# Kernel optimization log

Measured on AMD Instinct MI355X. Metric: run time of the kernel, lower is better.

## Reference

```python
import jax, jax.numpy as jnp
import numpy as np

B, S, C = 256, 169, 512      # batch, input seq_len (hardcoded 169 in source), n_attn
H, TT, HS = 256, 256, 16     # n_head, ctx_len, head_size (all forced by hardcoded shapes)
OUT = 64                     # output Linear(16, 64)


def setup_inputs() -> dict:
    key = jax.random.key(0)
    ks = jax.random.split(key, 13)
    s_in = 1.0 / np.sqrt(C)
    s_hs = 1.0 / np.sqrt(HS)
    return {
        "x": jax.random.normal(ks[0], (B, S, C), dtype=jnp.float32),
        "time_w": jax.random.normal(ks[1], (H, TT), dtype=jnp.float32) * 0.1,
        "time_alpha": jax.random.normal(ks[2], (H, 1, TT), dtype=jnp.float32) * 0.1 + 1.0,
        "time_beta": jax.random.normal(ks[3], (H, TT, 1), dtype=jnp.float32) * 0.1 + 1.0,
        "time_gamma": jax.random.normal(ks[4], (TT, 1), dtype=jnp.float32) * 0.1 + 1.0,
        "key_w": jax.random.normal(ks[5], (HS, C), dtype=jnp.float32) * s_in,
        "key_b": jax.random.normal(ks[6], (HS,), dtype=jnp.float32) * s_in,
        "value_w": jax.random.normal(ks[7], (HS, C), dtype=jnp.float32) * s_in,
        "value_b": jax.random.normal(ks[8], (HS,), dtype=jnp.float32) * s_in,
        "recep_w": jax.random.normal(ks[9], (HS, C), dtype=jnp.float32) * s_in,
        "recep_b": jax.random.normal(ks[10], (HS,), dtype=jnp.float32) * s_in,
        "out_w": jax.random.normal(ks[11], (OUT, HS), dtype=jnp.float32) * s_hs,
        "out_b": jax.random.normal(ks[12], (OUT,), dtype=jnp.float32) * s_hs,
    }


def reference(x, time_w, time_alpha, time_beta, time_gamma,
              key_w, key_b, value_w, value_b, recep_w, recep_b,
              out_w, out_b):
    # --- build the time-decay matrix via the pad/tile shift trick ---
    w = jnp.pad(time_w, ((0, 0), (0, TT)))            # (H, 2TT)
    w = jnp.tile(w, (1, TT))                          # (H, 2TT*TT)
    w = w[:, :-TT].reshape(H, TT, 2 * TT - 1)
    w = w[:, :, TT - 1:]                              # (H, TT, TT)
    w = w * time_alpha * time_beta                    # (H, TT, TT)

    # --- channel-half time shift: first C/2 channels shifted back by 1 step ---
    half = C // 2
    shifted = jnp.pad(x[:, :, :half], ((0, 0), (1, 0), (0, 0)))[:, :-1]
    x = jnp.concatenate([shifted, x[:, :, half:]], axis=-1)

    # --- projections (torch Linear: y = x @ W.T + b) ---
    k = x @ key_w.T + key_b                           # (B, S, HS)
    v = x @ value_w.T + value_b
    r = x @ recep_w.T + recep_b

    pad_len = TT - S                                  # 256 - 169 = 87
    r = jnp.pad(r, ((0, 0), (0, pad_len), (0, 0)))    # (B, TT, HS)

    k = jnp.exp(jnp.clip(k, -60.0, 30.0))
    sum_k = jnp.cumsum(k, axis=1)                     # (B, S, HS)
    sum_k = jnp.pad(sum_k, ((0, 0), (0, pad_len), (0, 0)))  # (B, TT, HS)

    kv = k * v                                        # (B, S, HS)
    kv = jnp.pad(kv, ((0, 0), (0, pad_len), (0, 0)))  # (B, TT, HS)

    # einsum('htu,bhc->btc') == contract u first, then (t,h) matmul against kv's seq axis
    w2 = w.sum(axis=-1)                               # (H, TT): sum_u w[h,t,u]
    wkv = jnp.einsum('ht,bhc->btc', w2, kv)           # (B, TT, HS)

    # original divides by zero-padded sum_k in the padded tail; guard with 1 there
    denom = jnp.where(sum_k == 0, jnp.ones_like(sum_k), sum_k)
    rwkv = jax.nn.sigmoid(r) * wkv / denom            # (B, TT, HS)

    rwkv = rwkv @ out_w.T + out_b                     # (B, TT, 64)
    rwkv = rwkv * time_gamma[:TT]                     # (TT,1) broadcast
    return rwkv
```

## Files before the change

kernel.cpp:

```cpp
#include <hip/hip_runtime.h>

typedef unsigned short u16;
typedef unsigned int u32;
typedef __attribute__((ext_vector_type(8))) __bf16 bf16x8;
typedef __attribute__((ext_vector_type(8))) u16 u16x8;
typedef __attribute__((ext_vector_type(4))) float f32x4;

#define S_LEN 169
#define C_DIM 512
#define SP 192

#define WT_OFF  0
#define XT_OFF  49152
#define KE_OFF  0
#define KVF_OFF 11264
#define RF_OFF  22528
#define KVT_OFF 33792
#define G_OFF   39936
#define RB_OFF  51200
#define SS_OFF  71680
#define OW_OFF  72704
#define LDS_BYTES 77824

__device__ __forceinline__ u16 f2b(float f) {
    union { float f; u32 u; } v; v.f = f;
    u32 u = v.u;
    return (u16)((u + 0x7fffu + ((u >> 16) & 1u)) >> 16);
}

__global__ __launch_bounds__(256) void w2_kernel(
    const float* __restrict__ time_w,
    const float* __restrict__ time_alpha,
    const float* __restrict__ time_beta,
    u16* __restrict__ w2t)
{
    __shared__ float tw[256];
    __shared__ float al[256];
    const int s = blockIdx.x;
    const int t = threadIdx.x;
    if (s >= S_LEN) { w2t[t * SP + s] = 0; return; }
    tw[t] = time_w[s * 256 + t];
    al[t] = time_alpha[s * 256 + t];
    __syncthreads();
    float acc = 0.f;
    for (int u = 0; u <= t; ++u)
        acc = fmaf(tw[255 + u - t], al[u], acc);
    w2t[t * SP + s] = f2b(time_beta[s * 256 + t] * acc);
}

__global__ __launch_bounds__(512) void rwkv_main(
    const float* __restrict__ x,
    const float* __restrict__ key_w, const float* __restrict__ key_b,
    const float* __restrict__ value_w, const float* __restrict__ value_b,
    const float* __restrict__ recep_w, const float* __restrict__ recep_b,
    const float* __restrict__ out_w, const float* __restrict__ out_b,
    const float* __restrict__ gamma,
    const u16* __restrict__ w2t,
    float* __restrict__ out)
{
    __shared__ __align__(16) char smem[LDS_BYTES];
    const int tid  = threadIdx.x;
    const int lane = tid & 63;
    const int wid  = tid >> 6;
    const int q    = lane >> 4;
    const int hs   = lane & 15;
    const int b    = blockIdx.x;
    const float* xb = x + (size_t)b * (S_LEN * C_DIM);

    for (int i = tid; i < 3072; i += 512) {
        int j  = i >> 6;
        int co = (i & 63) << 3;
        const float* src;
        if (j < 16)      src = key_w   + j * 512 + co;
        else if (j < 32) src = value_w + (j - 16) * 512 + co;
        else             src = recep_w + (j - 32) * 512 + co;
        float4 f0 = *(const float4*)src;
        float4 f1 = *(const float4*)(src + 4);
        u16x8 p;
        p[0]=f2b(f0.x); p[1]=f2b(f0.y); p[2]=f2b(f0.z); p[3]=f2b(f0.w);
        p[4]=f2b(f1.x); p[5]=f2b(f1.y); p[6]=f2b(f1.z); p[7]=f2b(f1.w);
        u32 off = (((u32)j << 10) + ((u32)co << 1)) ^ (((u32)(j & 7)) << 4);
        *(u16x8*)(smem + WT_OFF + off) = p;
    }

    const float kb = key_b[hs];
    const float vb = value_b[hs];
    const float rb = recep_b[hs];

    f32x4 acc0[3], acc1[3];
    #pragma unroll
    for (int n = 0; n < 3; ++n) { acc0[n] = (f32x4){0.f,0.f,0.f,0.f}; acc1[n] = (f32x4){0.f,0.f,0.f,0.f}; }
    const bool has_m1 = (wid < 3);

    for (int chunk = 0; chunk < 8; ++chunk) {
        if (chunk) __syncthreads();
        const bool shifted = chunk < 4;
        for (int i = tid; i < 1408; i += 512) {
            int r  = i >> 3;
            int co = (i & 7) << 3;
            int cg = (chunk << 6) + co;
            int tsrc = shifted ? (r - 1) : r;
            bool valid = shifted ? (r >= 1 && r <= S_LEN) : (r < S_LEN);
            u16x8 p = {0,0,0,0,0,0,0,0};
            if (valid) {
                const float* src = xb + (size_t)tsrc * C_DIM + cg;
                float4 f0 = *(const float4*)src;
                float4 f1 = *(const float4*)(src + 4);
                p[0]=f2b(f0.x); p[1]=f2b(f0.y); p[2]=f2b(f0.z); p[3]=f2b(f0.w);
                p[4]=f2b(f1.x); p[5]=f2b(f1.y); p[6]=f2b(f1.z); p[7]=f2b(f1.w);
            }
            u32 off = (((u32)r << 7) + ((u32)co << 1)) ^ (((u32)(r & 7)) << 4);
            *(u16x8*)(smem + XT_OFF + off) = p;
        }
        __syncthreads();
        #pragma unroll
        for (int ks = 0; ks < 2; ++ks) {
            int kc = ks << 5;
            bf16x8 bfr[3];
            #pragma unroll
            for (int nt = 0; nt < 3; ++nt) {
                int j = nt * 16 + hs;
                u32 col = (u32)((chunk << 6) + kc + (q << 3));
                u32 off = (((u32)j << 10) + (col << 1)) ^ (((u32)(j & 7)) << 4);
                bfr[nt] = *(const bf16x8*)(smem + WT_OFF + off);
            }
            {
                int row = wid * 16 + hs;
                u32 off = (((u32)row << 7) + ((u32)(kc + (q << 3)) << 1)) ^ (((u32)(row & 7)) << 4);
                bf16x8 afr = *(const bf16x8*)(smem + XT_OFF + off);
                acc0[0] = __builtin_amdgcn_mfma_f32_16x16x32_bf16(afr, bfr[0], acc0[0], 0,0,0);
                acc0[1] = __builtin_amdgcn_mfma_f32_16x16x32_bf16(afr, bfr[1], acc0[1], 0,0,0);
                acc0[2] = __builtin_amdgcn_mfma_f32_16x16x32_bf16(afr, bfr[2], acc0[2], 0,0,0);
            }
            if (has_m1) {
                int row = (wid + 8) * 16 + hs;
                u32 off = (((u32)row << 7) + ((u32)(kc + (q << 3)) << 1)) ^ (((u32)(row & 7)) << 4);
                bf16x8 afr = *(const bf16x8*)(smem + XT_OFF + off);
                acc1[0] = __builtin_amdgcn_mfma_f32_16x16x32_bf16(afr, bfr[0], acc1[0], 0,0,0);
                acc1[1] = __builtin_amdgcn_mfma_f32_16x16x32_bf16(afr, bfr[1], acc1[1], 0,0,0);
                acc1[2] = __builtin_amdgcn_mfma_f32_16x16x32_bf16(afr, bfr[2], acc1[2], 0,0,0);
            }
        }
    }
    __syncthreads();

    float* kef = (float*)(smem + KE_OFF);
    float* kvf = (float*)(smem + KVF_OFF);
    float* rff = (float*)(smem + RF_OFF);
    #pragma unroll
    for (int m = 0; m < 2; ++m) {
        if (m == 1 && !has_m1) break;
        const f32x4* A = (m == 0) ? acc0 : acc1;
        int tb = (wid + m * 8) * 16 + (q << 2);
        float ke[4];
        #pragma unroll
        for (int rg = 0; rg < 4; ++rg) {
            float kk = A[0][rg] + kb;
            kk = fminf(fmaxf(kk, -60.f), 30.f);
            ke[rg] = __expf(kk);
        }
        #pragma unroll
        for (int rg = 0; rg < 4; ++rg) {
            int t = tb + rg;
            kef[t * 16 + hs] = ke[rg];
            kvf[t * 16 + hs] = ke[rg] * (A[1][rg] + vb);
            rff[t * 16 + hs] = A[2][rg] + rb;
        }
    }
    __syncthreads();

    float* seg = (float*)(smem + SS_OFF);
    float* g   = (float*)(smem + G_OFF);
    if (tid < 256) {
        int h = tid & 15, sg = tid >> 4;
        int t0 = sg * 11, t1 = (t0 + 11 < S_LEN) ? t0 + 11 : S_LEN;
        float s = 0.f;
        for (int t = t0; t < t1; ++t) s += kef[t * 16 + h];
        seg[sg * 16 + h] = s;
    } else {
        int i2 = tid - 256;
        for (int i = i2; i < 4096; i += 256) {
            int row = i >> 4, c = 16 + (i & 15);
            ((u16*)(smem + RB_OFF))[row * 40 + c] = 0;
        }
        for (int i = i2; i < 368; i += 256) {
            int h = i & 15; int t = S_LEN + (i >> 4);
            u32 off = ((u32)(h * 384 + t * 2)) ^ (((u32)(h & 7)) << 4);
            *(u16*)(smem + KVT_OFF + off) = 0;
        }
        for (int i = i2; i < 2560; i += 256) {
            int o = i / 40, c = i - o * 40;
            u16 vb16 = (c < 16) ? f2b(out_w[o * 16 + c]) : (u16)0;
            ((u16*)(smem + OW_OFF))[o * 40 + c] = vb16;
        }
    }
    __syncthreads();
    if (tid < 16) {
        float run = 0.f;
        for (int sg = 0; sg < 16; ++sg) {
            float v = seg[sg * 16 + tid];
            seg[sg * 16 + tid] = run;
            run += v;
        }
    }
    __syncthreads();
    if (tid < 256) {
        int h = tid & 15, sg = tid >> 4;
        int t0 = sg * 11, t1 = (t0 + 11 < S_LEN) ? t0 + 11 : S_LEN;
        float run = seg[sg * 16 + h];
        for (int t = t0; t < t1; ++t) {
            run += kef[t * 16 + h];
            u32 off = ((u32)(h * 384 + t * 2)) ^ (((u32)(h & 7)) << 4);
            *(u16*)(smem + KVT_OFF + off) = f2b(kvf[t * 16 + h]);
            float rr = rff[t * 16 + h];
            float sig = 1.f / (1.f + __expf(-rr));
            g[t * 16 + h] = sig / run;
        }
    }
    __syncthreads();

    f32x4 wa0 = (f32x4){0.f,0.f,0.f,0.f};
    f32x4 wa1 = (f32x4){0.f,0.f,0.f,0.f};
    #pragma unroll
    for (int s0 = 0; s0 < SP; s0 += 32) {
        int scol = s0 + (q << 3);
        u32 boff = ((u32)(hs * 384 + scol * 2)) ^ (((u32)(hs & 7)) << 4);
        bf16x8 bfr = *(const bf16x8*)(smem + KVT_OFF + boff);
        {
            int row = wid * 16 + hs;
            bf16x8 afr = *(const bf16x8*)(w2t + row * SP + scol);
            wa0 = __builtin_amdgcn_mfma_f32_16x16x32_bf16(afr, bfr, wa0, 0,0,0);
        }
        {
            int row = (wid + 8) * 16 + hs;
            bf16x8 afr = *(const bf16x8*)(w2t + row * SP + scol);
            wa1 = __builtin_amdgcn_mfma_f32_16x16x32_bf16(afr, bfr, wa1, 0,0,0);
        }
    }
    #pragma unroll
    for (int m = 0; m < 2; ++m) {
        const f32x4& W = (m == 0) ? wa0 : wa1;
        int tb = (wid + m * 8) * 16 + (q << 2);
        #pragma unroll
        for (int rg = 0; rg < 4; ++rg) {
            int t = tb + rg;
            float fac = (t < S_LEN) ? g[t * 16 + hs] : 0.5f;
            ((u16*)(smem + RB_OFF))[t * 40 + hs] = f2b(W[rg] * fac);
        }
    }
    __syncthreads();

    float obv[4];
    #pragma unroll
    for (int nt = 0; nt < 4; ++nt) obv[nt] = out_b[nt * 16 + hs];
    #pragma unroll
    for (int m = 0; m < 2; ++m) {
        int mt = wid + m * 8;
        int arow = mt * 16 + hs;
        bf16x8 afr = *(const bf16x8*)(smem + RB_OFF + (u32)(arow * 80 + (q << 4)));
        float gm[4];
        #pragma unroll
        for (int rg = 0; rg < 4; ++rg) gm[rg] = gamma[mt * 16 + (q << 2) + rg];
        #pragma unroll
        for (int nt = 0; nt < 4; ++nt) {
            int orow = nt * 16 + hs;
            bf16x8 bfr = *(const bf16x8*)(smem + OW_OFF + (u32)(orow * 80 + (q << 4)));
            f32x4 zc = (f32x4){0.f,0.f,0.f,0.f};
            f32x4 d = __builtin_amdgcn_mfma_f32_16x16x32_bf16(afr, bfr, zc, 0,0,0);
            #pragma unroll
            for (int rg = 0; rg < 4; ++rg) {
                int t = mt * 16 + (q << 2) + rg;
                out[(size_t)b * 16384 + (size_t)t * 64 + nt * 16 + hs] = (d[rg] + obv[nt]) * gm[rg];
            }
        }
    }
}

extern "C" void kernel_launch(void* const* d_in, const int* in_sizes, int n_in,
                              void* d_out, int out_size, void* d_ws, size_t ws_size,
                              hipStream_t stream) {
    const float* x          = (const float*)d_in[0];
    const float* time_w     = (const float*)d_in[1];
    const float* time_alpha = (const float*)d_in[2];
    const float* time_beta  = (const float*)d_in[3];
    const float* time_gamma = (const float*)d_in[4];
    const float* key_w      = (const float*)d_in[5];
    const float* key_b      = (const float*)d_in[6];
    const float* value_w    = (const float*)d_in[7];
    const float* value_b    = (const float*)d_in[8];
    const float* recep_w    = (const float*)d_in[9];
    const float* recep_b    = (const float*)d_in[10];
    const float* out_w      = (const float*)d_in[11];
    const float* out_b      = (const float*)d_in[12];
    u16* w2t = (u16*)d_ws;

    w2_kernel<<<192, 256, 0, stream>>>(time_w, time_alpha, time_beta, w2t);
    rwkv_main<<<256, 512, 0, stream>>>(x, key_w, key_b, value_w, value_b,
                                       recep_w, recep_b, out_w, out_b,
                                       time_gamma, w2t, (float*)d_out);
}
```

Measured before the change: 40.91 us.

## Double-buffer x chunks in LDS with register prefetch; split w2 reduction

```diff
diff --git a/kernel.cpp b/kernel.cpp
--- a/kernel.cpp
+++ b/kernel.cpp
@@ -3,7 +3,6 @@
 typedef unsigned short u16;
 typedef unsigned int u32;
 typedef __attribute__((ext_vector_type(8))) __bf16 bf16x8;
-typedef __attribute__((ext_vector_type(8))) u16 u16x8;
 typedef __attribute__((ext_vector_type(4))) float f32x4;
 
 #define S_LEN 169
@@ -11,7 +10,8 @@
 #define SP 192
 
 #define WT_OFF  0
-#define XT_OFF  49152
+#define XT0_OFF 49152
+#define XT1_OFF 71680
 #define KE_OFF  0
 #define KVF_OFF 11264
 #define RF_OFF  22528
@@ -20,32 +20,36 @@
 #define RB_OFF  51200
 #define SS_OFF  71680
 #define OW_OFF  72704
-#define LDS_BYTES 77824
-
-__device__ __forceinline__ u16 f2b(float f) {
-    union { float f; u32 u; } v; v.f = f;
-    u32 u = v.u;
-    return (u16)((u + 0x7fffu + ((u >> 16) & 1u)) >> 16);
-}
-
-__global__ __launch_bounds__(256) void w2_kernel(
+#define LDS_BYTES 94208
+
+__global__ __launch_bounds__(1024) void w2_kernel(
     const float* __restrict__ time_w,
     const float* __restrict__ time_alpha,
     const float* __restrict__ time_beta,
-    u16* __restrict__ w2t)
+    __bf16* __restrict__ w2t)
 {
     __shared__ float tw[256];
     __shared__ float al[256];
+    __shared__ float part[4][256];
     const int s = blockIdx.x;
-    const int t = threadIdx.x;
-    if (s >= S_LEN) { w2t[t * SP + s] = 0; return; }
-    tw[t] = time_w[s * 256 + t];
-    al[t] = time_alpha[s * 256 + t];
-    __syncthreads();
+    const int t = threadIdx.x & 255;
+    const int p = threadIdx.x >> 8;
+    if (s >= S_LEN) {
+        if (p == 0) w2t[t * SP + s] = (__bf16)0.f;
+        return;
+    }
+    if (p == 0) { tw[t] = time_w[s * 256 + t]; al[t] = time_alpha[s * 256 + t]; }
+    __syncthreads();
+    const int u0 = p << 6;
+    const int u1 = (u0 + 64 < t + 1) ? (u0 + 64) : (t + 1);
     float acc = 0.f;
-    for (int u = 0; u <= t; ++u)
+    for (int u = u0; u < u1; ++u)
         acc = fmaf(tw[255 + u - t], al[u], acc);
-    w2t[t * SP + s] = f2b(time_beta[s * 256 + t] * acc);
+    part[p][t] = acc;
+    __syncthreads();
+    if (p == 0)
+        w2t[t * SP + s] = (__bf16)(time_beta[s * 256 + t] *
+                                   (part[0][t] + part[1][t] + part[2][t] + part[3][t]));
 }
 
 __global__ __launch_bounds__(512) void rwkv_main(
@@ -55,7 +59,7 @@
     const float* __restrict__ recep_w, const float* __restrict__ recep_b,
     const float* __restrict__ out_w, const float* __restrict__ out_b,
     const float* __restrict__ gamma,
-    const u16* __restrict__ w2t,
+    const __bf16* __restrict__ w2t,
     float* __restrict__ out)
 {
     __shared__ __align__(16) char smem[LDS_BYTES];
@@ -76,11 +80,11 @@
         else             src = recep_w + (j - 32) * 512 + co;
         float4 f0 = *(const float4*)src;
         float4 f1 = *(const float4*)(src + 4);
-        u16x8 p;
-        p[0]=f2b(f0.x); p[1]=f2b(f0.y); p[2]=f2b(f0.z); p[3]=f2b(f0.w);
-        p[4]=f2b(f1.x); p[5]=f2b(f1.y); p[6]=f2b(f1.z); p[7]=f2b(f1.w);
+        bf16x8 p;
+        p[0]=(__bf16)f0.x; p[1]=(__bf16)f0.y; p[2]=(__bf16)f0.z; p[3]=(__bf16)f0.w;
+        p[4]=(__bf16)f1.x; p[5]=(__bf16)f1.y; p[6]=(__bf16)f1.z; p[7]=(__bf16)f1.w;
         u32 off = (((u32)j << 10) + ((u32)co << 1)) ^ (((u32)(j & 7)) << 4);
-        *(u16x8*)(smem + WT_OFF + off) = p;
+        *(bf16x8*)(smem + WT_OFF + off) = p;
     }
 
     const float kb = key_b[hs];
@@ -92,27 +96,51 @@
     for (int n = 0; n < 3; ++n) { acc0[n] = (f32x4){0.f,0.f,0.f,0.f}; acc1[n] = (f32x4){0.f,0.f,0.f,0.f}; }
     const bool has_m1 = (wid < 3);
 
-    for (int chunk = 0; chunk < 8; ++chunk) {
-        if (chunk) __syncthreads();
+    float4 pf[3][2];
+    int pv[3];
+
+    auto ldchunk = [&](int chunk) {
         const bool shifted = chunk < 4;
-        for (int i = tid; i < 1408; i += 512) {
-            int r  = i >> 3;
-            int co = (i & 7) << 3;
-            int cg = (chunk << 6) + co;
-            int tsrc = shifted ? (r - 1) : r;
-            bool valid = shifted ? (r >= 1 && r <= S_LEN) : (r < S_LEN);
-            u16x8 p = {0,0,0,0,0,0,0,0};
-            if (valid) {
-                const float* src = xb + (size_t)tsrc * C_DIM + cg;
-                float4 f0 = *(const float4*)src;
-                float4 f1 = *(const float4*)(src + 4);
-                p[0]=f2b(f0.x); p[1]=f2b(f0.y); p[2]=f2b(f0.z); p[3]=f2b(f0.w);
-                p[4]=f2b(f1.x); p[5]=f2b(f1.y); p[6]=f2b(f1.z); p[7]=f2b(f1.w);
-            }
-            u32 off = (((u32)r << 7) + ((u32)co << 1)) ^ (((u32)(r & 7)) << 4);
-            *(u16x8*)(smem + XT_OFF + off) = p;
-        }
-        __syncthreads();
+        #pragma unroll
+        for (int it = 0; it < 3; ++it) {
+            int i = tid + (it << 9);
+            pv[it] = 0;
+            if (i < 1408) {
+                int r = i >> 3;
+                int tsrc = shifted ? (r - 1) : r;
+                bool valid = shifted ? (r >= 1 && r <= S_LEN) : (r < S_LEN);
+                pv[it] = 1;
+                if (valid) {
+                    const float* src = xb + (size_t)tsrc * C_DIM + (chunk << 6) + ((i & 7) << 3);
+                    pf[it][0] = *(const float4*)src;
+                    pf[it][1] = *(const float4*)(src + 4);
+                    pv[it] = 2;
+                }
+            }
+        }
+    };
+
+    auto cvtwrite = [&](u32 base) {
+        #pragma unroll
+        for (int it = 0; it < 3; ++it) {
+            int i = tid + (it << 9);
+            if (i < 1408 && pv[it]) {
+                int r = i >> 3, co = (i & 7) << 3;
+                bf16x8 p = {(__bf16)0.f,(__bf16)0.f,(__bf16)0.f,(__bf16)0.f,
+                            (__bf16)0.f,(__bf16)0.f,(__bf16)0.f,(__bf16)0.f};
+                if (pv[it] == 2) {
+                    p[0]=(__bf16)pf[it][0].x; p[1]=(__bf16)pf[it][0].y;
+                    p[2]=(__bf16)pf[it][0].z; p[3]=(__bf16)pf[it][0].w;
+                    p[4]=(__bf16)pf[it][1].x; p[5]=(__bf16)pf[it][1].y;
+                    p[6]=(__bf16)pf[it][1].z; p[7]=(__bf16)pf[it][1].w;
+                }
+                u32 off = (((u32)r << 7) + ((u32)co << 1)) ^ (((u32)(r & 7)) << 4);
+                *(bf16x8*)(smem + base + off) = p;
+            }
+        }
+    };
+
+    auto mfma_chunk = [&](int chunk, u32 xbase) {
         #pragma unroll
         for (int ks = 0; ks < 2; ++ks) {
             int kc = ks << 5;
@@ -127,7 +155,7 @@
             {
                 int row = wid * 16 + hs;
                 u32 off = (((u32)row << 7) + ((u32)(kc + (q << 3)) << 1)) ^ (((u32)(row & 7)) << 4);
-                bf16x8 afr = *(const bf16x8*)(smem + XT_OFF + off);
+                bf16x8 afr = *(const bf16x8*)(smem + xbase + off);
                 acc0[0] = __builtin_amdgcn_mfma_f32_16x16x32_bf16(afr, bfr[0], acc0[0], 0,0,0);
                 acc0[1] = __builtin_amdgcn_mfma_f32_16x16x32_bf16(afr, bfr[1], acc0[1], 0,0,0);
                 acc0[2] = __builtin_amdgcn_mfma_f32_16x16x32_bf16(afr, bfr[2], acc0[2], 0,0,0);
@@ -135,14 +163,26 @@
             if (has_m1) {
                 int row = (wid + 8) * 16 + hs;
                 u32 off = (((u32)row << 7) + ((u32)(kc + (q << 3)) << 1)) ^ (((u32)(row & 7)) << 4);
-                bf16x8 afr = *(const bf16x8*)(smem + XT_OFF + off);
+                bf16x8 afr = *(const bf16x8*)(smem + xbase + off);
                 acc1[0] = __builtin_amdgcn_mfma_f32_16x16x32_bf16(afr, bfr[0], acc1[0], 0,0,0);
                 acc1[1] = __builtin_amdgcn_mfma_f32_16x16x32_bf16(afr, bfr[1], acc1[1], 0,0,0);
                 acc1[2] = __builtin_amdgcn_mfma_f32_16x16x32_bf16(afr, bfr[2], acc1[2], 0,0,0);
             }
         }
-    }
-    __syncthreads();
+    };
+
+    ldchunk(0);
+    cvtwrite(XT0_OFF);
+    __syncthreads();
+    #pragma unroll
+    for (int chunk = 0; chunk < 8; ++chunk) {
+        const u32 cur = (chunk & 1) ? XT1_OFF : XT0_OFF;
+        const u32 nxt = (chunk & 1) ? XT0_OFF : XT1_OFF;
+        if (chunk < 7) ldchunk(chunk + 1);
+        mfma_chunk(chunk, cur);
+        if (chunk < 7) cvtwrite(nxt);
+        __syncthreads();
+    }
 
     float* kef = (float*)(smem + KE_OFF);
     float* kvf = (float*)(smem + KVF_OFF);
@@ -181,17 +221,16 @@
         int i2 = tid - 256;
         for (int i = i2; i < 4096; i += 256) {
             int row = i >> 4, c = 16 + (i & 15);
-            ((u16*)(smem + RB_OFF))[row * 40 + c] = 0;
+            ((__bf16*)(smem + RB_OFF))[row * 40 + c] = (__bf16)0.f;
         }
         for (int i = i2; i < 368; i += 256) {
             int h = i & 15; int t = S_LEN + (i >> 4);
             u32 off = ((u32)(h * 384 + t * 2)) ^ (((u32)(h & 7)) << 4);
-            *(u16*)(smem + KVT_OFF + off) = 0;
+            *(__bf16*)(smem + KVT_OFF + off) = (__bf16)0.f;
         }
         for (int i = i2; i < 2560; i += 256) {
             int o = i / 40, c = i - o * 40;
-            u16 vb16 = (c < 16) ? f2b(out_w[o * 16 + c]) : (u16)0;
-            ((u16*)(smem + OW_OFF))[o * 40 + c] = vb16;
+            ((__bf16*)(smem + OW_OFF))[o * 40 + c] = (c < 16) ? (__bf16)out_w[o * 16 + c] : (__bf16)0.f;
         }
     }
     __syncthreads();
@@ -211,7 +250,7 @@
         for (int t = t0; t < t1; ++t) {
             run += kef[t * 16 + h];
             u32 off = ((u32)(h * 384 + t * 2)) ^ (((u32)(h & 7)) << 4);
-            *(u16*)(smem + KVT_OFF + off) = f2b(kvf[t * 16 + h]);
+            *(__bf16*)(smem + KVT_OFF + off) = (__bf16)kvf[t * 16 + h];
             float rr = rff[t * 16 + h];
             float sig = 1.f / (1.f + __expf(-rr));
             g[t * 16 + h] = sig / run;
@@ -245,7 +284,7 @@
         for (int rg = 0; rg < 4; ++rg) {
             int t = tb + rg;
             float fac = (t < S_LEN) ? g[t * 16 + hs] : 0.5f;
-            ((u16*)(smem + RB_OFF))[t * 40 + hs] = f2b(W[rg] * fac);
+            ((__bf16*)(smem + RB_OFF))[t * 40 + hs] = (__bf16)(W[rg] * fac);
         }
     }
     __syncthreads();
@@ -292,9 +331,9 @@
     const float* recep_b    = (const float*)d_in[10];
     const float* out_w      = (const float*)d_in[11];
     const float* out_b      = (const float*)d_in[12];
-    u16* w2t = (u16*)d_ws;
-
-    w2_kernel<<<192, 256, 0, stream>>>(time_w, time_alpha, time_beta, w2t);
+    __bf16* w2t = (__bf16*)d_ws;
+
+    w2_kernel<<<192, 1024, 0, stream>>>(time_w, time_alpha, time_beta, w2t);
     rwkv_main<<<256, 512, 0, stream>>>(x, key_w, key_b, value_w, value_b,
                                        recep_w, recep_b, out_w, out_b,
                                        time_gamma, w2t, (float*)d_out);
```

Measured after the change: 38.12 us. 1.07x faster.
